# Optimization experiments

Hardware: AMD Instinct MI355X
Metric: run time of the kernel (lower is better)

The kernel has to match this reference:

```python
import jax, jax.numpy as jnp
import numpy as np
import math

B, S, HD, NH, L, FF = 8, 512, 768, 12, 12, 3072
DH = HD // NH
EPS = 1e-12
REL_BINS, MAX_REL = 32, 128
REL2D_BINS, MAX_REL2D = 64, 256


def rel_bucket(rel_pos, num_buckets, max_distance):
    # bidirectional bucketing, faithful to relative_position_bucket
    nb = num_buckets // 2
    ret = (rel_pos > 0).astype(jnp.int32) * nb
    n = jnp.abs(rel_pos).astype(jnp.int32)
    max_exact = nb // 2
    is_small = n < max_exact
    scale = (nb - max_exact) / math.log(max_distance / max_exact)
    val = max_exact + (jnp.log(jnp.maximum(n, 1).astype(jnp.float32) / max_exact) * scale).astype(jnp.int32)
    val = jnp.minimum(val, nb - 1)
    return ret + jnp.where(is_small, n, val)


def layernorm(x, g, b):
    m = jnp.mean(x, axis=-1, keepdims=True)
    v = jnp.var(x, axis=-1, keepdims=True)
    return (x - m) * jax.lax.rsqrt(v + EPS) * g + b


def setup_inputs() -> dict:
    key = jax.random.key(0)
    ks = jax.random.split(key, 12)
    r = lambda k, shape: jax.random.normal(k, shape, jnp.float32) * 0.02
    z = lambda shape: jnp.zeros(shape, jnp.float32)
    o = lambda shape: jnp.ones(shape, jnp.float32)
    return {
        'hidden_states': jax.random.normal(ks[0], (B, S, HD), jnp.float32),
        'attention_mask': jnp.zeros((B, 1, 1, S), jnp.bool_),  # True = masked
        'position_ids': jnp.broadcast_to(jnp.arange(S, dtype=jnp.int32), (B, S)),
        'bbox': jax.random.randint(ks[1], (B, S, 4), 0, 1000, dtype=jnp.int32),
        'qkv_w': r(ks[2], (L, HD, 3 * HD)),
        'q_bias': z((L, HD)), 'v_bias': z((L, HD)),
        'attn_out_w': r(ks[3], (L, HD, HD)), 'attn_out_b': z((L, HD)),
        'ln1_g': o((L, HD)), 'ln1_b': z((L, HD)),
        'inter_w': r(ks[4], (L, HD, FF)), 'inter_b': z((L, FF)),
        'out_w': r(ks[5], (L, FF, HD)), 'out_b': z((L, HD)),
        'ln2_g': o((L, HD)), 'ln2_b': z((L, HD)),
        'rel_pos_w': r(ks[6], (REL_BINS, NH)),
        'rel_x_w': r(ks[7], (REL2D_BINS, NH)),
        'rel_y_w': r(ks[8], (REL2D_BINS, NH)),
    }


def reference(hidden_states, attention_mask, position_ids, bbox,
              qkv_w, q_bias, v_bias, attn_out_w, attn_out_b, ln1_g, ln1_b,
              inter_w, inter_b, out_w, out_b, ln2_g, ln2_b,
              rel_pos_w, rel_x_w, rel_y_w):
    # ---- 1D relative position bias: [B, NH, S, S] ----
    rp = position_ids[:, None, :] - position_ids[:, :, None]  # mem - query
    rel_pos = rel_pos_w[rel_bucket(rp, REL_BINS, MAX_REL)]     # [B,S,S,NH]
    rel_pos = rel_pos.transpose(0, 3, 1, 2)
    # ---- 2D spatial bias from bbox x (col 0) and y (col 3) ----
    px, py = bbox[:, :, 0], bbox[:, :, 3]
    bx = rel_bucket(px[:, None, :] - px[:, :, None], REL2D_BINS, MAX_REL2D)
    by = rel_bucket(py[:, None, :] - py[:, :, None], REL2D_BINS, MAX_REL2D)
    rel_2d = (rel_x_w[bx] + rel_y_w[by]).transpose(0, 3, 1, 2)  # [B,NH,S,S]
    bias = rel_pos + rel_2d
    mask = attention_mask.astype(jnp.bool_)  # [B,1,1,S], True = masked
    inv_sqrt_dh = 1.0 / math.sqrt(DH)

    def heads(x):  # [B,S,HD] -> [B,NH,S,DH]
        return x.reshape(B, S, NH, DH).transpose(0, 2, 1, 3)

    def layer(h, p):
        qw, qb, vb, aow, aob, g1, b1, iw, ib, ow, ob, g2, b2 = p
        qkv = h @ qw  # fast_qkv, no bias on the fused linear
        q, k, v = jnp.split(qkv, 3, axis=-1)
        q = heads(q + qb) * inv_sqrt_dh
        k = heads(k)
        v = heads(v + vb)
        scores = jnp.einsum('bhsd,bhtd->bhst', q, k) + bias
        scores = jnp.where(mask, -jnp.inf, scores.astype(jnp.float32))
        probs = jax.nn.softmax(scores, axis=-1).astype(h.dtype)
        ctx = jnp.einsum('bhst,bhtd->bhsd', probs, v)
        ctx = ctx.transpose(0, 2, 1, 3).reshape(B, S, HD)
        attn = layernorm(ctx @ aow + aob + h, g1, b1)
        ffn = jax.nn.gelu(attn @ iw + ib, approximate=False)
        out = layernorm(ffn @ ow + ob + attn, g2, b2)
        return out, None

    params = (qkv_w, q_bias, v_bias, attn_out_w, attn_out_b, ln1_g, ln1_b,
              inter_w, inter_b, out_w, out_b, ln2_g, ln2_b)
    h, _ = jax.lax.scan(layer, hidden_states, params)
    return h
```

## Files before the change

kernel.cpp:

```cpp
#include <hip/hip_runtime.h>
#include <math.h>

typedef unsigned short u16;
typedef short bf16x8 __attribute__((ext_vector_type(8)));
typedef unsigned short u16x8 __attribute__((ext_vector_type(8)));
typedef float f32x4 __attribute__((ext_vector_type(4)));

#define L_  12
#define B_  8
#define S_  512
#define HD_ 768
#define NH_ 12
#define DH_ 64
#define FF_ 3072

__device__ __forceinline__ u16 f2bf(float f) {
    unsigned u = __float_as_uint(f);
    u += 0x7fffu + ((u >> 16) & 1u);
    return (u16)(u >> 16);
}
__device__ __forceinline__ float bf2f(u16 h) {
    return __uint_as_float(((unsigned)h) << 16);
}

__device__ __forceinline__ void ld_lds16(const u16* g, u16* l) {
    __builtin_amdgcn_global_load_lds((const __attribute__((address_space(1))) void*)g,
                                     (__attribute__((address_space(3))) void*)l, 16, 0, 0);
}

__device__ __forceinline__ int rel_bucket(int rel, int num_buckets, int max_distance) {
    int nb = num_buckets >> 1;
    int ret = (rel > 0) ? nb : 0;
    int n = abs(rel);
    int max_exact = nb >> 1;
    if (n < max_exact) return ret + n;
    float scale = (float)(nb - max_exact) / logf((float)max_distance / (float)max_exact);
    int val = max_exact + (int)(logf(fmaxf((float)n, 1.0f) / (float)max_exact) * scale);
    val = min(val, nb - 1);
    return ret + val;
}

__global__ __launch_bounds__(256) void transpose_k(const float* __restrict__ in,
                                                   u16* __restrict__ out, int K, int N) {
    __shared__ u16 tile[32][33];
    const int k0 = blockIdx.x * 32, n0 = blockIdx.y * 32;
    const int tx = threadIdx.x & 31, ty = threadIdx.x >> 5;
#pragma unroll
    for (int r = 0; r < 32; r += 8)
        tile[ty + r][tx] = f2bf(in[(long)(k0 + ty + r) * N + n0 + tx]);
    __syncthreads();
#pragma unroll
    for (int r = 0; r < 32; r += 8)
        out[(long)(n0 + ty + r) * K + k0 + tx] = tile[tx][ty + r];
}

__global__ __launch_bounds__(256) void bucket_k(const int* __restrict__ pos,
                                                const int* __restrict__ bbox,
                                                unsigned* __restrict__ out) {
    const int bi = blockIdx.x;
    const int b = bi >> 9;
    const int t = threadIdx.x;
    const int pos_i = pos[bi];
    const int px_i = bbox[bi * 4 + 0];
    const int py_i = bbox[bi * 4 + 3];
    for (int j = t; j < S_; j += 256) {
        int bp = rel_bucket(pos[b * S_ + j] - pos_i, 32, 128);
        int bx = rel_bucket(bbox[(b * S_ + j) * 4 + 0] - px_i, 64, 256);
        int by = rel_bucket(bbox[(b * S_ + j) * 4 + 3] - py_i, 64, 256);
        out[((long)bi << 9) + j] = (unsigned)bp | ((unsigned)bx << 8) | ((unsigned)by << 16);
    }
}

__global__ __launch_bounds__(256) void bias_k(const unsigned* __restrict__ bk,
                                              const float* __restrict__ rpw,
                                              const float* __restrict__ rxw,
                                              const float* __restrict__ ryw,
                                              u16* __restrict__ out) {
    __shared__ float tb[1920];
    const int t = threadIdx.x;
    for (int i = t; i < 384; i += 256) tb[i] = rpw[i];
    for (int i = t; i < 768; i += 256) { tb[384 + i] = rxw[i]; tb[1152 + i] = ryw[i]; }
    __syncthreads();
    const int bi = blockIdx.x;
    const int b = bi >> 9, i = bi & 511;
    const unsigned* br = bk + ((long)bi << 9);
    for (int idx = t; idx < NH_ * S_; idx += 256) {
        const int h = idx >> 9, j = idx & 511;
        unsigned kk = br[j];
        float v = tb[(kk & 255) * 12 + h] + tb[384 + ((kk >> 8) & 255) * 12 + h] +
                  tb[1152 + ((kk >> 16) & 255) * 12 + h];
        out[((long)(b * NH_ + h) * S_ + i) * S_ + j] = f2bf(v);
    }
}

__global__ __launch_bounds__(256) void init_k(const float* __restrict__ hs,
                                              float* __restrict__ h, u16* __restrict__ hb) {
    const int i = blockIdx.x * 256 + threadIdx.x;
    float v = hs[i];
    h[i] = v;
    hb[i] = f2bf(v);
}

template <int EPI>
__global__ __launch_bounds__(256) void gemm128_k(
    const u16* __restrict__ A, const u16* __restrict__ Bt, int N, int K, int Kc,
    long zStride,
    const float* __restrict__ bias, const float* __restrict__ bias2,
    float* __restrict__ outF,
    u16* __restrict__ oB0, u16* __restrict__ oB1, u16* __restrict__ oB2) {
    __shared__ __align__(16) u16 As[128 * 32];
    __shared__ __align__(16) u16 Bs[128 * 32];
    const int tid = threadIdx.x;
    const int wave = tid >> 6, lane = tid & 63;
    const int lrow = lane & 15, quad = lane >> 4;
    const int wr = wave >> 1, wc = wave & 1;
    const long zoff = (long)blockIdx.z * Kc;
    const u16* Ag = A + (long)blockIdx.x * 128 * K + (long)(tid >> 2) * K + ((tid & 3) << 3) + zoff;
    const u16* Bg = Bt + (long)blockIdx.y * 128 * K + (long)(tid >> 2) * K + ((tid & 3) << 3) + zoff;
    const long rs64 = (long)64 * K;
    u16* Al = As + tid * 8;
    u16* Bl = Bs + tid * 8;
    f32x4 acc[4][4] = {};
    for (int k0 = 0; k0 < Kc; k0 += 32) {
        ld_lds16(Ag + k0, Al);
        ld_lds16(Ag + rs64 + k0, Al + 2048);
        ld_lds16(Bg + k0, Bl);
        ld_lds16(Bg + rs64 + k0, Bl + 2048);
        __syncthreads();
        bf16x8 a[4], b[4];
#pragma unroll
        for (int i = 0; i < 4; i++)
            a[i] = *(const bf16x8*)(As + (wr * 64 + i * 16 + lrow) * 32 + (quad << 3));
#pragma unroll
        for (int j = 0; j < 4; j++)
            b[j] = *(const bf16x8*)(Bs + (wc * 64 + j * 16 + lrow) * 32 + (quad << 3));
#pragma unroll
        for (int i = 0; i < 4; i++)
#pragma unroll
            for (int j = 0; j < 4; j++)
                acc[i][j] = __builtin_amdgcn_mfma_f32_16x16x32_bf16(a[i], b[j], acc[i][j], 0, 0, 0);
        __syncthreads();
    }
    const int rbase = blockIdx.x * 128 + wr * 64 + (quad << 2);
    const int cbase = blockIdx.y * 128 + wc * 64 + lrow;
    const bool addb = (blockIdx.z == 0);
#pragma unroll
    for (int i = 0; i < 4; i++) {
#pragma unroll
        for (int j = 0; j < 4; j++) {
            const int gc = cbase + j * 16;
#pragma unroll
            for (int r = 0; r < 4; r++) {
                const int gr = rbase + i * 16 + r;
                float v = acc[i][j][r];
                if (EPI == 0) {
                    if (addb) v += bias[gc];
                    outF[(long)blockIdx.z * zStride + (long)gr * N + gc] = v;
                } else if (EPI == 1) {
                    v += bias[gc];
                    v = 0.5f * v * (1.0f + erff(v * 0.70710678118654752f));
                    oB0[(long)gr * N + gc] = f2bf(v);
                } else {
                    int b = gr >> 9, s = gr & 511;
                    int part = gc / HD_;
                    int cm = gc - part * HD_;
                    int hh = cm >> 6, d = cm & 63;
                    long hb = (long)(b * NH_ + hh);
                    if (part == 0) {
                        float q = (v + bias[cm]) * 0.125f;
                        oB0[(hb * S_ + s) * DH_ + d] = f2bf(q);
                    } else if (part == 1) {
                        oB1[(hb * S_ + s) * DH_ + d] = f2bf(v);
                    } else {
                        oB2[(hb * DH_ + d) * S_ + s] = f2bf(v + bias2[cm]);
                    }
                }
            }
        }
    }
}

template <bool USEB>
__global__ __launch_bounds__(256, 3) void attn_fused_k(
    const u16* __restrict__ q, const u16* __restrict__ k, const u16* __restrict__ vt,
    const u16* __restrict__ bias, const unsigned* __restrict__ bk,
    const float* __restrict__ rpw, const float* __restrict__ rxw,
    const float* __restrict__ ryw, u16* __restrict__ ctx) {
    __shared__ float tb[1920];
    __shared__ __align__(16) u16 Pw[4][2048];
    const int t = threadIdx.x;
    if constexpr (!USEB) {
        for (int i = t; i < 384; i += 256) tb[i] = rpw[i];
        for (int i = t; i < 768; i += 256) { tb[384 + i] = rxw[i]; tb[1152 + i] = ryw[i]; }
    }
    const int wv = t >> 6, lane = t & 63;
    const int lrow = lane & 15, quad = lane >> 4;
    const int bh = blockIdx.y, b = bh / NH_, h = bh - b * NH_;
    const int qt = blockIdx.x;
    const int q0 = qt * 64 + wv * 16;
    const u16* qb = q + ((long)bh * S_ + q0 + lrow) * DH_ + (quad << 3);
    const u16* kb = k + ((long)bh * S_ + lrow) * DH_ + (quad << 3);
    bf16x8 qf0 = *(const bf16x8*)qb;
    bf16x8 qf1 = *(const bf16x8*)(qb + 32);
    if constexpr (!USEB) __syncthreads();
    f32x4 acc[32];
#pragma unroll
    for (int ct = 0; ct < 32; ct++) {
        const u16* kp = kb + (long)(ct * 16) * DH_;
        bf16x8 k0 = *(const bf16x8*)kp;
        bf16x8 k1 = *(const bf16x8*)(kp + 32);
        f32x4 z = {0.f, 0.f, 0.f, 0.f};
        z = __builtin_amdgcn_mfma_f32_16x16x32_bf16(k0, qf0, z, 0, 0, 0);
        acc[ct] = __builtin_amdgcn_mfma_f32_16x16x32_bf16(k1, qf1, z, 0, 0, 0);
    }
    float m = -1e30f;
    if constexpr (USEB) {
        const u16* bb = bias + ((long)bh * S_ + q0 + lrow) * S_ + (quad << 2);
#pragma unroll
        for (int ct = 0; ct < 32; ct++) {
            ushort4 b4 = *(const ushort4*)(bb + ct * 16);
            acc[ct][0] += bf2f(b4.x);
            acc[ct][1] += bf2f(b4.y);
            acc[ct][2] += bf2f(b4.z);
            acc[ct][3] += bf2f(b4.w);
            m = fmaxf(m, fmaxf(fmaxf(acc[ct][0], acc[ct][1]), fmaxf(acc[ct][2], acc[ct][3])));
        }
    } else {
        const unsigned* br = bk + ((long)(b * S_ + q0 + lrow) << 9) + (quad << 2);
#pragma unroll
        for (int ct = 0; ct < 32; ct++) {
            uint4 k4 = *(const uint4*)(br + ct * 16);
            unsigned ka[4] = {k4.x, k4.y, k4.z, k4.w};
#pragma unroll
            for (int r = 0; r < 4; r++) {
                unsigned kk = ka[r];
                acc[ct][r] += tb[(kk & 255) * 12 + h] + tb[384 + ((kk >> 8) & 255) * 12 + h] +
                              tb[1152 + ((kk >> 16) & 255) * 12 + h];
            }
            m = fmaxf(m, fmaxf(fmaxf(acc[ct][0], acc[ct][1]), fmaxf(acc[ct][2], acc[ct][3])));
        }
    }
    m = fmaxf(m, __shfl_xor(m, 16));
    m = fmaxf(m, __shfl_xor(m, 32));
    float s = 0.f;
#pragma unroll
    for (int ct = 0; ct < 32; ct++) {
#pragma unroll
        for (int r = 0; r < 4; r++) {
            float e = __expf(acc[ct][r] - m);
            acc[ct][r] = e;
            s += e;
        }
    }
    s += __shfl_xor(s, 16);
    s += __shfl_xor(s, 32);
    const float inv = 1.0f / s;
    f32x4 o[4] = {};
    const u16* vb = vt + ((long)bh * DH_ + lrow) * S_ + (quad << 3);
    u16* pw = &Pw[wv][0];
    const int wg = quad >> 1;
    const int wbyte = (quad & 1) << 3;
    const int rsw = lrow & 7;
#pragma unroll
    for (int c = 0; c < 4; c++) {
        asm volatile("s_waitcnt lgkmcnt(0)" ::: "memory");
        __builtin_amdgcn_sched_barrier(0);
#pragma unroll
        for (int lc = 0; lc < 8; lc++) {
            const f32x4 a = acc[c * 8 + lc];
            ushort4 pk;
            pk.x = f2bf(a[0] * inv);
            pk.y = f2bf(a[1] * inv);
            pk.z = f2bf(a[2] * inv);
            pk.w = f2bf(a[3] * inv);
            const int g = lc * 2 + wg;
            *(ushort4*)((char*)pw + lrow * 256 + (((g ^ rsw)) << 4) + wbyte) = pk;
        }
        asm volatile("s_waitcnt lgkmcnt(0)" ::: "memory");
        __builtin_amdgcn_sched_barrier(0);
#pragma unroll
        for (int ss = 0; ss < 4; ss++) {
            bf16x8 ap = *(const bf16x8*)((char*)pw + lrow * 256 +
                                         ((((ss << 2) + quad) ^ rsw) << 4));
            const u16* vp = vb + c * 128 + ss * 32;
#pragma unroll
            for (int dt = 0; dt < 4; dt++) {
                bf16x8 bv = *(const bf16x8*)(vp + (long)(dt * 16) * S_);
                o[dt] = __builtin_amdgcn_mfma_f32_16x16x32_bf16(ap, bv, o[dt], 0, 0, 0);
            }
        }
    }
    u16* cb = ctx + ((long)(b * S_ + qt * 64 + wv * 16 + (quad << 2))) * HD_ + h * DH_ + lrow;
#pragma unroll
    for (int dt = 0; dt < 4; dt++)
#pragma unroll
        for (int i = 0; i < 4; i++)
            cb[(long)i * HD_ + dt * 16] = f2bf(o[dt][i]);
}

__global__ __launch_bounds__(256) void ln_k(const float* __restrict__ x0,
                                            const float* __restrict__ x1,
                                            const float* __restrict__ res,
                                            const float* __restrict__ g,
                                            const float* __restrict__ b,
                                            float* __restrict__ outF,
                                            u16* __restrict__ outB) {
    const long row = blockIdx.x;
    const float* xr = x0 + row * HD_;
    const float* yr = x1 + row * HD_;
    const float* rr = res + row * HD_;
    const int t = threadIdx.x;
    float v0 = xr[t] + yr[t] + rr[t];
    float v1 = xr[t + 256] + yr[t + 256] + rr[t + 256];
    float v2 = xr[t + 512] + yr[t + 512] + rr[t + 512];
    __shared__ float red[256];
    red[t] = v0 + v1 + v2;
    __syncthreads();
    for (int o = 128; o > 0; o >>= 1) {
        if (t < o) red[t] += red[t + o];
        __syncthreads();
    }
    float mean = red[0] * (1.0f / 768.0f);
    __syncthreads();
    float d0 = v0 - mean, d1 = v1 - mean, d2 = v2 - mean;
    red[t] = d0 * d0 + d1 * d1 + d2 * d2;
    __syncthreads();
    for (int o = 128; o > 0; o >>= 1) {
        if (t < o) red[t] += red[t + o];
        __syncthreads();
    }
    float rstd = rsqrtf(red[0] * (1.0f / 768.0f) + 1e-12f);
    float y0 = d0 * rstd * g[t] + b[t];
    float y1 = d1 * rstd * g[t + 256] + b[t + 256];
    float y2 = d2 * rstd * g[t + 512] + b[t + 512];
    outF[row * HD_ + t] = y0;
    outF[row * HD_ + t + 256] = y1;
    outF[row * HD_ + t + 512] = y2;
    outB[row * HD_ + t] = f2bf(y0);
    outB[row * HD_ + t + 256] = f2bf(y1);
    outB[row * HD_ + t + 512] = f2bf(y2);
}

extern "C" void kernel_launch(void* const* d_in, const int* in_sizes, int n_in,
                              void* d_out, int out_size, void* d_ws, size_t ws_size,
                              hipStream_t stream) {
    const float* hs     = (const float*)d_in[0];
    const int*   pos    = (const int*)d_in[2];
    const int*   bbox   = (const int*)d_in[3];
    const float* qkv_w  = (const float*)d_in[4];
    const float* q_bias = (const float*)d_in[5];
    const float* v_bias = (const float*)d_in[6];
    const float* aow    = (const float*)d_in[7];
    const float* aob    = (const float*)d_in[8];
    const float* g1     = (const float*)d_in[9];
    const float* b1     = (const float*)d_in[10];
    const float* iw     = (const float*)d_in[11];
    const float* ib     = (const float*)d_in[12];
    const float* ow     = (const float*)d_in[13];
    const float* ob     = (const float*)d_in[14];
    const float* g2     = (const float*)d_in[15];
    const float* b2     = (const float*)d_in[16];
    const float* rpw    = (const float*)d_in[17];
    const float* rxw    = (const float*)d_in[18];
    const float* ryw    = (const float*)d_in[19];

    char* wp = (char*)d_ws;
    auto take = [&](size_t bytes) -> char* {
        char* p = wp;
        wp += (bytes + 255) & ~(size_t)255;
        return p;
    };
    u16*   wq     = (u16*)take((size_t)2304 * 768 * 2);
    u16*   wa     = (u16*)take((size_t)768 * 768 * 2);
    u16*   wiT    = (u16*)take((size_t)3072 * 768 * 2);
    u16*   woT    = (u16*)take((size_t)768 * 3072 * 2);
    unsigned* buckets = (unsigned*)take((size_t)B_ * S_ * S_ * 4);
    char*  regA   = take((size_t)B_ * NH_ * S_ * S_ * 2);
    float* tmpF   = (float*)regA;
    float* tmpF2  = (float*)(regA + (size_t)B_ * S_ * HD_ * 4);
    u16*   ffnb   = (u16*)(regA + (size_t)2 * B_ * S_ * HD_ * 4);
    u16*   qbuf   = (u16*)take((size_t)B_ * NH_ * S_ * DH_ * 2);
    u16*   kbuf   = (u16*)take((size_t)B_ * NH_ * S_ * DH_ * 2);
    u16*   vtbuf  = (u16*)take((size_t)B_ * NH_ * S_ * DH_ * 2);
    u16*   hbf    = (u16*)take((size_t)B_ * S_ * HD_ * 2);
    u16*   ctxb   = (u16*)take((size_t)B_ * S_ * HD_ * 2);
    float* attnF  = (float*)take((size_t)B_ * S_ * HD_ * 4);
    u16*   attnB  = (u16*)take((size_t)B_ * S_ * HD_ * 2);
    char*  base_end = wp;
    u16*   biasT  = (u16*)take((size_t)B_ * NH_ * S_ * S_ * 2);

    if ((size_t)(base_end - (char*)d_ws) > ws_size) return;
    const bool useBias = (size_t)(wp - (char*)d_ws) <= ws_size;

    dim3 blk(256);
    float* hout = (float*)d_out;
    const long ZS = (long)4096 * 768;

    bucket_k<<<dim3(B_ * S_), blk, 0, stream>>>(pos, bbox, buckets);
    init_k<<<dim3((B_ * S_ * HD_) / 256), blk, 0, stream>>>(hs, hout, hbf);
    if (useBias)
        bias_k<<<dim3(B_ * S_), blk, 0, stream>>>(buckets, rpw, rxw, ryw, biasT);

    for (int l = 0; l < L_; l++) {
        transpose_k<<<dim3(24, 72), blk, 0, stream>>>(qkv_w + (size_t)l * 768 * 2304, wq, 768, 2304);
        transpose_k<<<dim3(24, 24), blk, 0, stream>>>(aow + (size_t)l * 768 * 768, wa, 768, 768);
        transpose_k<<<dim3(24, 96), blk, 0, stream>>>(iw + (size_t)l * 768 * 3072, wiT, 768, 3072);
        transpose_k<<<dim3(96, 24), blk, 0, stream>>>(ow + (size_t)l * 3072 * 768, woT, 3072, 768);

        gemm128_k<2><<<dim3(32, 18, 1), blk, 0, stream>>>(
            hbf, wq, 2304, 768, 768, 0L, q_bias + l * HD_, v_bias + l * HD_,
            nullptr, qbuf, kbuf, vtbuf);

        if (useBias)
            attn_fused_k<true><<<dim3(8, 96), blk, 0, stream>>>(
                qbuf, kbuf, vtbuf, biasT, buckets, rpw, rxw, ryw, ctxb);
        else
            attn_fused_k<false><<<dim3(8, 96), blk, 0, stream>>>(
                qbuf, kbuf, vtbuf, nullptr, buckets, rpw, rxw, ryw, ctxb);

        gemm128_k<0><<<dim3(32, 6, 2), blk, 0, stream>>>(
            ctxb, wa, 768, 768, 384, ZS, aob + l * HD_, nullptr,
            tmpF, nullptr, nullptr, nullptr);

        ln_k<<<dim3(B_ * S_), blk, 0, stream>>>(tmpF, tmpF2, hout,
                                                g1 + l * HD_, b1 + l * HD_, attnF, attnB);

        gemm128_k<1><<<dim3(32, 24, 1), blk, 0, stream>>>(
            attnB, wiT, 3072, 768, 768, 0L, ib + l * FF_, nullptr,
            nullptr, ffnb, nullptr, nullptr);

        gemm128_k<0><<<dim3(32, 6, 2), blk, 0, stream>>>(
            ffnb, woT, 768, 3072, 1536, ZS, ob + l * HD_, nullptr,
            tmpF, nullptr, nullptr, nullptr);

        ln_k<<<dim3(B_ * S_), blk, 0, stream>>>(tmpF, tmpF2, attnF,
                                                g2 + l * HD_, b2 + l * HD_, hout, hbf);
    }
}
```

Before: 3.385 ms.

## Batch weight transposes across layers and stream attention softmax online over key tiles

```diff
diff --git a/kernel.cpp b/kernel.cpp
--- a/kernel.cpp
+++ b/kernel.cpp
@@ -42,6 +42,9 @@
 
 __global__ __launch_bounds__(256) void transpose_k(const float* __restrict__ in,
                                                    u16* __restrict__ out, int K, int N) {
+    const size_t zo = (size_t)blockIdx.z * K * N;
+    in += zo;
+    out += zo;
     __shared__ u16 tile[32][33];
     const int k0 = blockIdx.x * 32, n0 = blockIdx.y * 32;
     const int tx = threadIdx.x & 31, ty = threadIdx.x >> 5;
@@ -180,19 +183,11 @@
     }
 }
 
-template <bool USEB>
-__global__ __launch_bounds__(256, 3) void attn_fused_k(
+__global__ __launch_bounds__(256) void attn_fused_k(
     const u16* __restrict__ q, const u16* __restrict__ k, const u16* __restrict__ vt,
-    const u16* __restrict__ bias, const unsigned* __restrict__ bk,
-    const float* __restrict__ rpw, const float* __restrict__ rxw,
-    const float* __restrict__ ryw, u16* __restrict__ ctx) {
-    __shared__ float tb[1920];
+    const u16* __restrict__ bias, u16* __restrict__ ctx) {
     __shared__ __align__(16) u16 Pw[4][2048];
     const int t = threadIdx.x;
-    if constexpr (!USEB) {
-        for (int i = t; i < 384; i += 256) tb[i] = rpw[i];
-        for (int i = t; i < 768; i += 256) { tb[384 + i] = rxw[i]; tb[1152 + i] = ryw[i]; }
-    }
     const int wv = t >> 6, lane = t & 63;
     const int lrow = lane & 15, quad = lane >> 4;
     const int bh = blockIdx.y, b = bh / NH_, h = bh - b * NH_;
@@ -200,102 +195,90 @@
     const int q0 = qt * 64 + wv * 16;
     const u16* qb = q + ((long)bh * S_ + q0 + lrow) * DH_ + (quad << 3);
     const u16* kb = k + ((long)bh * S_ + lrow) * DH_ + (quad << 3);
+    const u16* bb = bias + ((long)bh * S_ + q0 + lrow) * S_ + (quad << 2);
+    const u16* vb = vt + ((long)bh * DH_ + lrow) * S_ + (quad << 3);
     bf16x8 qf0 = *(const bf16x8*)qb;
     bf16x8 qf1 = *(const bf16x8*)(qb + 32);
-    if constexpr (!USEB) __syncthreads();
-    f32x4 acc[32];
-#pragma unroll
-    for (int ct = 0; ct < 32; ct++) {
-        const u16* kp = kb + (long)(ct * 16) * DH_;
-        bf16x8 k0 = *(const bf16x8*)kp;
-        bf16x8 k1 = *(const bf16x8*)(kp + 32);
-        f32x4 z = {0.f, 0.f, 0.f, 0.f};
-        z = __builtin_amdgcn_mfma_f32_16x16x32_bf16(k0, qf0, z, 0, 0, 0);
-        acc[ct] = __builtin_amdgcn_mfma_f32_16x16x32_bf16(k1, qf1, z, 0, 0, 0);
-    }
-    float m = -1e30f;
-    if constexpr (USEB) {
-        const u16* bb = bias + ((long)bh * S_ + q0 + lrow) * S_ + (quad << 2);
-#pragma unroll
-        for (int ct = 0; ct < 32; ct++) {
-            ushort4 b4 = *(const ushort4*)(bb + ct * 16);
-            acc[ct][0] += bf2f(b4.x);
-            acc[ct][1] += bf2f(b4.y);
-            acc[ct][2] += bf2f(b4.z);
-            acc[ct][3] += bf2f(b4.w);
-            m = fmaxf(m, fmaxf(fmaxf(acc[ct][0], acc[ct][1]), fmaxf(acc[ct][2], acc[ct][3])));
-        }
-    } else {
-        const unsigned* br = bk + ((long)(b * S_ + q0 + lrow) << 9) + (quad << 2);
-#pragma unroll
-        for (int ct = 0; ct < 32; ct++) {
-            uint4 k4 = *(const uint4*)(br + ct * 16);
-            unsigned ka[4] = {k4.x, k4.y, k4.z, k4.w};
-#pragma unroll
-            for (int r = 0; r < 4; r++) {
-                unsigned kk = ka[r];
-                acc[ct][r] += tb[(kk & 255) * 12 + h] + tb[384 + ((kk >> 8) & 255) * 12 + h] +
-                              tb[1152 + ((kk >> 16) & 255) * 12 + h];
-            }
-            m = fmaxf(m, fmaxf(fmaxf(acc[ct][0], acc[ct][1]), fmaxf(acc[ct][2], acc[ct][3])));
-        }
-    }
-    m = fmaxf(m, __shfl_xor(m, 16));
-    m = fmaxf(m, __shfl_xor(m, 32));
-    float s = 0.f;
-#pragma unroll
-    for (int ct = 0; ct < 32; ct++) {
-#pragma unroll
-        for (int r = 0; r < 4; r++) {
-            float e = __expf(acc[ct][r] - m);
-            acc[ct][r] = e;
-            s += e;
-        }
-    }
-    s += __shfl_xor(s, 16);
-    s += __shfl_xor(s, 32);
-    const float inv = 1.0f / s;
-    f32x4 o[4] = {};
-    const u16* vb = vt + ((long)bh * DH_ + lrow) * S_ + (quad << 3);
     u16* pw = &Pw[wv][0];
     const int wg = quad >> 1;
     const int wbyte = (quad & 1) << 3;
     const int rsw = lrow & 7;
-#pragma unroll
-    for (int c = 0; c < 4; c++) {
-        asm volatile("s_waitcnt lgkmcnt(0)" ::: "memory");
-        __builtin_amdgcn_sched_barrier(0);
+
+    float m = -1e30f, s = 0.f;
+    f32x4 o[4] = {};
+#pragma unroll
+    for (int kt = 0; kt < 4; kt++) {
+        f32x4 acc[8];
 #pragma unroll
         for (int lc = 0; lc < 8; lc++) {
-            const f32x4 a = acc[c * 8 + lc];
+            const u16* kp = kb + (long)((kt * 8 + lc) * 16) * DH_;
+            bf16x8 k0 = *(const bf16x8*)kp;
+            bf16x8 k1 = *(const bf16x8*)(kp + 32);
+            f32x4 z = {0.f, 0.f, 0.f, 0.f};
+            z = __builtin_amdgcn_mfma_f32_16x16x32_bf16(k0, qf0, z, 0, 0, 0);
+            acc[lc] = __builtin_amdgcn_mfma_f32_16x16x32_bf16(k1, qf1, z, 0, 0, 0);
+        }
+        float pm = -1e30f;
+#pragma unroll
+        for (int lc = 0; lc < 8; lc++) {
+            ushort4 b4 = *(const ushort4*)(bb + (kt * 8 + lc) * 16);
+            acc[lc][0] += bf2f(b4.x);
+            acc[lc][1] += bf2f(b4.y);
+            acc[lc][2] += bf2f(b4.z);
+            acc[lc][3] += bf2f(b4.w);
+            pm = fmaxf(pm, fmaxf(fmaxf(acc[lc][0], acc[lc][1]), fmaxf(acc[lc][2], acc[lc][3])));
+        }
+        pm = fmaxf(pm, __shfl_xor(pm, 16));
+        pm = fmaxf(pm, __shfl_xor(pm, 32));
+        const float mn = fmaxf(m, pm);
+        const float f = __expf(m - mn);
+        m = mn;
+        s *= f;
+        float fr[4];
+#pragma unroll
+        for (int i = 0; i < 4; i++) fr[i] = __shfl(f, (quad << 2) + i);
+#pragma unroll
+        for (int dt = 0; dt < 4; dt++) {
+            o[dt][0] *= fr[0]; o[dt][1] *= fr[1]; o[dt][2] *= fr[2]; o[dt][3] *= fr[3];
+        }
+#pragma unroll
+        for (int lc = 0; lc < 8; lc++) {
+            float e0 = __expf(acc[lc][0] - mn);
+            float e1 = __expf(acc[lc][1] - mn);
+            float e2 = __expf(acc[lc][2] - mn);
+            float e3 = __expf(acc[lc][3] - mn);
+            s += e0 + e1 + e2 + e3;
             ushort4 pk;
-            pk.x = f2bf(a[0] * inv);
-            pk.y = f2bf(a[1] * inv);
-            pk.z = f2bf(a[2] * inv);
-            pk.w = f2bf(a[3] * inv);
+            pk.x = f2bf(e0); pk.y = f2bf(e1); pk.z = f2bf(e2); pk.w = f2bf(e3);
             const int g = lc * 2 + wg;
-            *(ushort4*)((char*)pw + lrow * 256 + (((g ^ rsw)) << 4) + wbyte) = pk;
-        }
-        asm volatile("s_waitcnt lgkmcnt(0)" ::: "memory");
-        __builtin_amdgcn_sched_barrier(0);
+            *(ushort4*)((char*)pw + lrow * 256 + ((g ^ rsw) << 4) + wbyte) = pk;
+        }
+        __builtin_amdgcn_sched_barrier(0x7F);
 #pragma unroll
         for (int ss = 0; ss < 4; ss++) {
             bf16x8 ap = *(const bf16x8*)((char*)pw + lrow * 256 +
                                          ((((ss << 2) + quad) ^ rsw) << 4));
-            const u16* vp = vb + c * 128 + ss * 32;
+            const u16* vp = vb + kt * 128 + ss * 32;
 #pragma unroll
             for (int dt = 0; dt < 4; dt++) {
                 bf16x8 bv = *(const bf16x8*)(vp + (long)(dt * 16) * S_);
                 o[dt] = __builtin_amdgcn_mfma_f32_16x16x32_bf16(ap, bv, o[dt], 0, 0, 0);
             }
         }
-    }
+        __builtin_amdgcn_sched_barrier(0x7F);
+    }
+    s += __shfl_xor(s, 16);
+    s += __shfl_xor(s, 32);
+    const float inv = 1.0f / s;
+    float invr[4];
+#pragma unroll
+    for (int i = 0; i < 4; i++) invr[i] = __shfl(inv, (quad << 2) + i);
     u16* cb = ctx + ((long)(b * S_ + qt * 64 + wv * 16 + (quad << 2))) * HD_ + h * DH_ + lrow;
 #pragma unroll
     for (int dt = 0; dt < 4; dt++)
 #pragma unroll
         for (int i = 0; i < 4; i++)
-            cb[(long)i * HD_ + dt * 16] = f2bf(o[dt][i]);
+            cb[(long)i * HD_ + dt * 16] = f2bf(o[dt][i] * invr[i]);
 }
 
 __global__ __launch_bounds__(256) void ln_k(const float* __restrict__ x0,
@@ -370,10 +353,10 @@
         wp += (bytes + 255) & ~(size_t)255;
         return p;
     };
-    u16*   wq     = (u16*)take((size_t)2304 * 768 * 2);
-    u16*   wa     = (u16*)take((size_t)768 * 768 * 2);
-    u16*   wiT    = (u16*)take((size_t)3072 * 768 * 2);
-    u16*   woT    = (u16*)take((size_t)768 * 3072 * 2);
+    u16*   wq     = (u16*)take((size_t)L_ * 2304 * 768 * 2);
+    u16*   wa     = (u16*)take((size_t)L_ * 768 * 768 * 2);
+    u16*   wiT    = (u16*)take((size_t)L_ * 3072 * 768 * 2);
+    u16*   woT    = (u16*)take((size_t)L_ * 768 * 3072 * 2);
     unsigned* buckets = (unsigned*)take((size_t)B_ * S_ * S_ * 4);
     char*  regA   = take((size_t)B_ * NH_ * S_ * S_ * 2);
     float* tmpF   = (float*)regA;
@@ -386,11 +369,9 @@
     u16*   ctxb   = (u16*)take((size_t)B_ * S_ * HD_ * 2);
     float* attnF  = (float*)take((size_t)B_ * S_ * HD_ * 4);
     u16*   attnB  = (u16*)take((size_t)B_ * S_ * HD_ * 2);
-    char*  base_end = wp;
     u16*   biasT  = (u16*)take((size_t)B_ * NH_ * S_ * S_ * 2);
 
-    if ((size_t)(base_end - (char*)d_ws) > ws_size) return;
-    const bool useBias = (size_t)(wp - (char*)d_ws) <= ws_size;
+    if ((size_t)(wp - (char*)d_ws) > ws_size) return;
 
     dim3 blk(256);
     float* hout = (float*)d_out;
@@ -398,39 +379,38 @@
 
     bucket_k<<<dim3(B_ * S_), blk, 0, stream>>>(pos, bbox, buckets);
     init_k<<<dim3((B_ * S_ * HD_) / 256), blk, 0, stream>>>(hs, hout, hbf);
-    if (useBias)
-        bias_k<<<dim3(B_ * S_), blk, 0, stream>>>(buckets, rpw, rxw, ryw, biasT);
+    bias_k<<<dim3(B_ * S_), blk, 0, stream>>>(buckets, rpw, rxw, ryw, biasT);
+
+    transpose_k<<<dim3(24, 72, L_), blk, 0, stream>>>(qkv_w, wq, 768, 2304);
+    transpose_k<<<dim3(24, 24, L_), blk, 0, stream>>>(aow, wa, 768, 768);
+    transpose_k<<<dim3(24, 96, L_), blk, 0, stream>>>(iw, wiT, 768, 3072);
+    transpose_k<<<dim3(96, 24, L_), blk, 0, stream>>>(ow, woT, 3072, 768);
 
     for (int l = 0; l < L_; l++) {
-        transpose_k<<<dim3(24, 72), blk, 0, stream>>>(qkv_w + (size_t)l * 768 * 2304, wq, 768, 2304);
-        transpose_k<<<dim3(24, 24), blk, 0, stream>>>(aow + (size_t)l * 768 * 768, wa, 768, 768);
-        transpose_k<<<dim3(24, 96), blk, 0, stream>>>(iw + (size_t)l * 768 * 3072, wiT, 768, 3072);
-        transpose_k<<<dim3(96, 24), blk, 0, stream>>>(ow + (size_t)l * 3072 * 768, woT, 3072, 768);
+        const u16* wq_l  = wq  + (size_t)l * 2304 * 768;
+        const u16* wa_l  = wa  + (size_t)l * 768 * 768;
+        const u16* wiT_l = wiT + (size_t)l * 3072 * 768;
+        const u16* woT_l = woT + (size_t)l * 768 * 3072;
 
         gemm128_k<2><<<dim3(32, 18, 1), blk, 0, stream>>>(
-            hbf, wq, 2304, 768, 768, 0L, q_bias + l * HD_, v_bias + l * HD_,
+            hbf, wq_l, 2304, 768, 768, 0L, q_bias + l * HD_, v_bias + l * HD_,
             nullptr, qbuf, kbuf, vtbuf);
 
-        if (useBias)
-            attn_fused_k<true><<<dim3(8, 96), blk, 0, stream>>>(
-                qbuf, kbuf, vtbuf, biasT, buckets, rpw, rxw, ryw, ctxb);
-        else
-            attn_fused_k<false><<<dim3(8, 96), blk, 0, stream>>>(
-                qbuf, kbuf, vtbuf, nullptr, buckets, rpw, rxw, ryw, ctxb);
+        attn_fused_k<<<dim3(8, 96), blk, 0, stream>>>(qbuf, kbuf, vtbuf, biasT, ctxb);
 
         gemm128_k<0><<<dim3(32, 6, 2), blk, 0, stream>>>(
-            ctxb, wa, 768, 768, 384, ZS, aob + l * HD_, nullptr,
+            ctxb, wa_l, 768, 768, 384, ZS, aob + l * HD_, nullptr,
             tmpF, nullptr, nullptr, nullptr);
 
         ln_k<<<dim3(B_ * S_), blk, 0, stream>>>(tmpF, tmpF2, hout,
                                                 g1 + l * HD_, b1 + l * HD_, attnF, attnB);
 
         gemm128_k<1><<<dim3(32, 24, 1), blk, 0, stream>>>(
-            attnB, wiT, 3072, 768, 768, 0L, ib + l * FF_, nullptr,
+            attnB, wiT_l, 3072, 768, 768, 0L, ib + l * FF_, nullptr,
             nullptr, ffnb, nullptr, nullptr);
 
         gemm128_k<0><<<dim3(32, 6, 2), blk, 0, stream>>>(
-            ffnb, woT, 768, 3072, 1536, ZS, ob + l * HD_, nullptr,
+            ffnb, woT_l, 768, 3072, 1536, ZS, ob + l * HD_, nullptr,
             tmpF, nullptr, nullptr, nullptr);
 
         ln_k<<<dim3(B_ * S_), blk, 0, stream>>>(tmpF, tmpF2, attnF,
```

Result: slower. 3.588 ms (+6.0%).
